# Kernel optimization log

Measured on AMD Instinct MI355X. Metric: run time of the kernel, lower is better.

## Reference

```python
import jax, jax.numpy as jnp
import numpy as np

ALPHA = 0.2  # LeakyReLU negative slope


def setup_inputs() -> dict:
    key = jax.random.key(0)
    k1, k2, k3, k4 = jax.random.split(key, 4)
    N, F_in, F_out = 8192, 128, 64
    x = jax.random.normal(k1, (N, F_in), dtype=jnp.float32)
    w = jax.random.normal(k2, (F_in, F_out), dtype=jnp.float32) * (1.0 / np.sqrt(F_in))
    a = jax.random.normal(k3, (2 * F_out, 1), dtype=jnp.float32) * (1.0 / np.sqrt(2 * F_out))
    adj_mat = jax.random.randint(k4, (N, N), 0, 2, dtype=jnp.int32)
    return {"x": x, "adj_mat": adj_mat, "w": w, "a": a}


def reference(x, adj_mat, w, a):
    # wh: [N, F_out]
    wh = x @ w
    F_out = w.shape[1]
    # The original builds a_input[i,j] = concat(wh[i], wh[j]) and dots with a.
    # Equivalently: e[i,j] = wh[i]@a[:F] + wh[j]@a[F:], computed without the
    # O(N^2 * 2F) concat tensor.
    src = wh @ a[:F_out, 0]   # [N]
    dst = wh @ a[F_out:, 0]   # [N]
    e = jax.nn.leaky_relu(src[:, None] + dst[None, :], negative_slope=ALPHA)  # [N,N]
    # NOTE: original masks non-edges with 0.0 (1e-12*zeros == 0), not -inf.
    attn = jnp.where(adj_mat > 0, e, jnp.zeros((), dtype=e.dtype))
    attn = jax.nn.softmax(attn, axis=1)
    h_prime = attn @ wh       # [N, F_out]
    return jax.nn.elu(h_prime)
```

## Files before the change

### kernel.cpp

```cpp
#include <hip/hip_runtime.h>
#include <hip/hip_bf16.h>


constexpr int N_ROWS = 8192;
constexpr int F_IN   = 128;
constexpr int F_OUT  = 64;
#define LRELU_A 0.2f
#define LOG2E   1.4426950408889634f

constexpr size_t OFF_WHT  = 0;
constexpr size_t OFF_SRC  = 1048576;
constexpr size_t OFF_DST  = OFF_SRC + 32768;
constexpr size_t OFF_LP   = OFF_DST + 32768;
constexpr size_t OFF_ACC  = OFF_LP + 16 * 32768;

typedef __attribute__((ext_vector_type(4))) float f32x4;
typedef __attribute__((ext_vector_type(4))) int   i32x4;
typedef __attribute__((ext_vector_type(8))) short s16x8;

static __device__ __forceinline__ short f2bf(float f) {
  unsigned u = __float_as_uint(f);
  u = (u + 0x7fffu + ((u >> 16) & 1u)) >> 16;
  return (short)u;
}

__global__ __launch_bounds__(256) void k1_proj(
    const float* __restrict__ x, const float* __restrict__ w,
    const float* __restrict__ a, short* __restrict__ whT,
    float* __restrict__ src, float* __restrict__ dst)
{
  const int lane = threadIdx.x & 63;
  const int wid  = threadIdx.x >> 6;
  const int rowBase = blockIdx.x * 32 + wid * 8;

  float acc[8];
#pragma unroll
  for (int r = 0; r < 8; ++r) acc[r] = 0.0f;

#pragma unroll 1
  for (int kc = 0; kc < 4; ++kc) {
    float wreg[32];
#pragma unroll
    for (int kk = 0; kk < 32; ++kk)
      wreg[kk] = w[(kc * 32 + kk) * F_OUT + lane];
#pragma unroll
    for (int r = 0; r < 8; ++r) {
      const f32x4* xp = (const f32x4*)(x + (size_t)(rowBase + r) * F_IN + kc * 32);
#pragma unroll
      for (int q = 0; q < 8; ++q) {
        f32x4 xv = xp[q];
        acc[r] = fmaf(xv.x, wreg[4*q+0], acc[r]);
        acc[r] = fmaf(xv.y, wreg[4*q+1], acc[r]);
        acc[r] = fmaf(xv.z, wreg[4*q+2], acc[r]);
        acc[r] = fmaf(xv.w, wreg[4*q+3], acc[r]);
      }
    }
  }

  s16x8 hb;
#pragma unroll
  for (int r = 0; r < 8; ++r) hb[r] = f2bf(acc[r]);
  *(s16x8*)&whT[(size_t)lane * N_ROWS + rowBase] = hb;

  const float aS = a[lane];
  const float aD = a[F_OUT + lane];
#pragma unroll
  for (int r = 0; r < 8; ++r) {
    float ts = acc[r] * aS;
    float td = acc[r] * aD;
#pragma unroll
    for (int off = 32; off > 0; off >>= 1) {
      ts += __shfl_xor(ts, off, 64);
      td += __shfl_xor(td, off, 64);
    }
    if (lane == 0) {
      src[rowBase + r] = ts * LOG2E;
      dst[rowBase + r] = td * LOG2E;
    }
  }
}

template<int S>
__global__ __launch_bounds__(512, 2) void k2_attn(
    const int* __restrict__ adj, const short* __restrict__ whT,
    const float* __restrict__ src, const float* __restrict__ dst,
    float* __restrict__ acc_part, float* __restrict__ l_part)
{
  constexpr int JLEN = N_ROWS / S;
  constexpr int NI   = JLEN / 64;
  __shared__ short Blds[64 * JLEN];
  __shared__ float Dlds[JLEN];

  const int tid  = threadIdx.x;
  const int lane = tid & 63;
  const int wid  = tid >> 6;
  const int s    = blockIdx.y;
  const int jbase = s * JLEN;
  const int rowg = blockIdx.x * 128 + wid * 16;
  const int r16  = lane & 15;
  const int kq   = lane >> 4;

#pragma unroll
  for (int q = 0; q < 8; ++q) {
    const int m   = tid + q * 512;
    const int f   = m >> 6;
    const int c16 = m & 63;
    const s16x8 v = *(const s16x8*)(whT + (size_t)f * N_ROWS + jbase + c16 * 8);
    *(s16x8*)((char*)Blds + f * (JLEN * 2) + ((c16 * 16) ^ ((f & 7) << 4))) = v;
  }
  if (tid < JLEN / 4)
    *(f32x4*)&Dlds[tid * 4] = *(const f32x4*)(dst + jbase + tid * 4);
  __syncthreads();

  const size_t arow = (size_t)(rowg + r16) * N_ROWS;
  const float sv = src[rowg + r16];
  const int cb0 = jbase + kq * 8;
  const int cswz = (r16 & 7) << 4;

  f32x4 acc0 = {0,0,0,0}, acc1 = {0,0,0,0}, acc2 = {0,0,0,0}, acc3 = {0,0,0,0};
  float lp = 0.0f;

  i32x4 A[3][4];

  auto issueAdj = [&](int b, int i) {
    const int* p = adj + arow + cb0 + i * 64;
    A[b][0] = *(const i32x4*)(p);
    A[b][1] = *(const i32x4*)(p + 4);
    A[b][2] = *(const i32x4*)(p + 32);
    A[b][3] = *(const i32x4*)(p + 36);
  };

  issueAdj(0, 0); issueAdj(1, 1); issueAdj(2, 2);

#pragma unroll
  for (int i = 0; i < NI; ++i) {
#pragma unroll
    for (int h = 0; h < 2; ++h) {
      const int db = kq * 8 + i * 64 + h * 32;
      const f32x4 dA = *(const f32x4*)&Dlds[db];
      const f32x4 dB = *(const f32x4*)&Dlds[db + 4];
      const i32x4 aA = A[i % 3][2 * h];
      const i32x4 aB = A[i % 3][2 * h + 1];
      float p0, p1, p2, p3, p4, p5, p6, p7;
#define PE(pp, dd, aa) { float e = sv + (dd); e = fmaxf(e, LRELU_A * e); \
                         (pp) = ((aa) > 0) ? __builtin_amdgcn_exp2f(e) : 1.0f; }
      PE(p0, dA.x, aA.x) PE(p1, dA.y, aA.y) PE(p2, dA.z, aA.z) PE(p3, dA.w, aA.w)
      PE(p4, dB.x, aB.x) PE(p5, dB.y, aB.y) PE(p6, dB.z, aB.z) PE(p7, dB.w, aB.w)
#undef PE
      lp += ((p0 + p1) + (p2 + p3)) + ((p4 + p5) + (p6 + p7));
      union { s16x8 v; __hip_bfloat16 b[8]; } u;
      u.b[0] = __float2bfloat16(p0); u.b[1] = __float2bfloat16(p1);
      u.b[2] = __float2bfloat16(p2); u.b[3] = __float2bfloat16(p3);
      u.b[4] = __float2bfloat16(p4); u.b[5] = __float2bfloat16(p5);
      u.b[6] = __float2bfloat16(p6); u.b[7] = __float2bfloat16(p7);
      const char* bb = (const char*)Blds;
      const int colb = (i * 64 + h * 32 + kq * 8) * 2;
      const s16x8 b0 = *(const s16x8*)(bb + (0 * 16 + r16) * (JLEN * 2) + (colb ^ cswz));
      const s16x8 b1 = *(const s16x8*)(bb + (1 * 16 + r16) * (JLEN * 2) + (colb ^ cswz));
      const s16x8 b2 = *(const s16x8*)(bb + (2 * 16 + r16) * (JLEN * 2) + (colb ^ cswz));
      const s16x8 b3 = *(const s16x8*)(bb + (3 * 16 + r16) * (JLEN * 2) + (colb ^ cswz));
      acc0 = __builtin_amdgcn_mfma_f32_16x16x32_bf16(u.v, b0, acc0, 0, 0, 0);
      acc1 = __builtin_amdgcn_mfma_f32_16x16x32_bf16(u.v, b1, acc1, 0, 0, 0);
      acc2 = __builtin_amdgcn_mfma_f32_16x16x32_bf16(u.v, b2, acc2, 0, 0, 0);
      acc3 = __builtin_amdgcn_mfma_f32_16x16x32_bf16(u.v, b3, acc3, 0, 0, 0);
    }
    if (i + 3 < NI) issueAdj(i % 3, i + 3);
  }

  lp += __shfl_xor(lp, 16, 64);
  lp += __shfl_xor(lp, 32, 64);
  if (lane < 16) l_part[(size_t)s * N_ROWS + rowg + lane] = lp;

#define STORE_ACC(av, nt) _Pragma("unroll") \
  for (int rg = 0; rg < 4; ++rg) { \
    const int row = rowg + kq * 4 + rg; \
    acc_part[((size_t)s * N_ROWS + row) * F_OUT + (nt) * 16 + r16] = (av)[rg]; \
  }
  STORE_ACC(acc0, 0) STORE_ACC(acc1, 1) STORE_ACC(acc2, 2) STORE_ACC(acc3, 3)
#undef STORE_ACC
}

template<int S>
__global__ __launch_bounds__(256) void k3_combine(
    const float* __restrict__ acc_part, const float* __restrict__ l_part,
    float* __restrict__ out)
{
  const int idx = blockIdx.x * 256 + threadIdx.x;
  const int row = idx >> 4;
  const int f4  = idx & 15;
  f32x4 h = {0.f, 0.f, 0.f, 0.f};
  float l = 0.f;
#pragma unroll
  for (int s = 0; s < S; ++s) {
    h += *(const f32x4*)(acc_part + ((size_t)s * N_ROWS + row) * F_OUT + 4 * f4);
    l += l_part[(size_t)s * N_ROWS + row];
  }
  const float inv = 1.0f / l;
  f32x4 o;
  {
    float v0 = h.x * inv; o.x = v0 > 0.f ? v0 : (__expf(v0) - 1.0f);
    float v1 = h.y * inv; o.y = v1 > 0.f ? v1 : (__expf(v1) - 1.0f);
    float v2 = h.z * inv; o.z = v2 > 0.f ? v2 : (__expf(v2) - 1.0f);
    float v3 = h.w * inv; o.w = v3 > 0.f ? v3 : (__expf(v3) - 1.0f);
  }
  *(f32x4*)(out + (size_t)row * F_OUT + 4 * f4) = o;
}

extern "C" void kernel_launch(void* const* d_in, const int* in_sizes, int n_in,
                              void* d_out, int out_size, void* d_ws, size_t ws_size,
                              hipStream_t stream) {
  const float* x   = (const float*)d_in[0];
  const int*   adj = (const int*)d_in[1];
  const float* w   = (const float*)d_in[2];
  const float* a   = (const float*)d_in[3];
  float* out = (float*)d_out;
  char* ws = (char*)d_ws;

  short* whT      = (short*)(ws + OFF_WHT);
  float* src      = (float*)(ws + OFF_SRC);
  float* dst      = (float*)(ws + OFF_DST);
  float* l_part   = (float*)(ws + OFF_LP);
  float* acc_part = (float*)(ws + OFF_ACC);

  k1_proj<<<N_ROWS / 32, 256, 0, stream>>>(x, w, a, whT, src, dst);
  k2_attn<16><<<dim3(N_ROWS / 128, 16), 512, 0, stream>>>(adj, whT, src, dst,
                                                          acc_part, l_part);
  k3_combine<16><<<(N_ROWS * F_OUT / 4) / 256, 256, 0, stream>>>(acc_part, l_part, out);
}
```

Measured before the change: 91.81 us.

## Coalesce adjacency loads via LDS staging of probabilities and smaller blocks

Each lane now loads contiguous 16-byte chunks of adjacency rows in a row-major pattern (8 lanes per row), so global reads of the dominant adj matrix are better coalesced. The computed probabilities are written to a per-wave LDS tile and re-read in MFMA A-operand layout. Blocks shrink from 512 to 256 threads (64 rows), doubling the grid, and each block now reloads the whT slice. This adds LDS round-trips and duplicate B-tile loads per block in exchange for memory-access efficiency on the bandwidth-bound adj stream.

```diff
diff --git a/kernel.cpp b/kernel.cpp
--- a/kernel.cpp
+++ b/kernel.cpp
@@ -16,6 +16,7 @@
 
 typedef __attribute__((ext_vector_type(4))) float f32x4;
 typedef __attribute__((ext_vector_type(4))) int   i32x4;
+typedef __attribute__((ext_vector_type(4))) short s16x4;
 typedef __attribute__((ext_vector_type(8))) short s16x8;
 
 static __device__ __forceinline__ short f2bf(float f) {
@@ -81,28 +82,32 @@
 }
 
 template<int S>
-__global__ __launch_bounds__(512, 2) void k2_attn(
+__global__ __launch_bounds__(256, 2) void k2_attn(
     const int* __restrict__ adj, const short* __restrict__ whT,
     const float* __restrict__ src, const float* __restrict__ dst,
     float* __restrict__ acc_part, float* __restrict__ l_part)
 {
   constexpr int JLEN = N_ROWS / S;
   constexpr int NI   = JLEN / 64;
+  constexpr int PSTR = 144;
   __shared__ short Blds[64 * JLEN];
   __shared__ float Dlds[JLEN];
+  __shared__ short Plds[4][16 * (PSTR / 2)];
 
   const int tid  = threadIdx.x;
   const int lane = tid & 63;
   const int wid  = tid >> 6;
   const int s    = blockIdx.y;
   const int jbase = s * JLEN;
-  const int rowg = blockIdx.x * 128 + wid * 16;
+  const int rowg = blockIdx.x * 64 + wid * 16;
   const int r16  = lane & 15;
   const int kq   = lane >> 4;
-
-#pragma unroll
-  for (int q = 0; q < 8; ++q) {
-    const int m   = tid + q * 512;
+  const int lg   = lane >> 3;
+  const int lc   = lane & 7;
+
+#pragma unroll
+  for (int q = 0; q < 16; ++q) {
+    const int m   = tid + q * 256;
     const int f   = m >> 6;
     const int c16 = m & 63;
     const s16x8 v = *(const s16x8*)(whT + (size_t)f * N_ROWS + jbase + c16 * 8);
@@ -112,64 +117,73 @@
     *(f32x4*)&Dlds[tid * 4] = *(const f32x4*)(dst + jbase + tid * 4);
   __syncthreads();
 
-  const size_t arow = (size_t)(rowg + r16) * N_ROWS;
-  const float sv = src[rowg + r16];
-  const int cb0 = jbase + kq * 8;
+  const size_t rbA = (size_t)(rowg + lg) * N_ROWS + jbase + lc * 4;
+  const size_t rbB = rbA + (size_t)8 * N_ROWS;
+  const float srcA = src[rowg + lg];
+  const float srcB = src[rowg + 8 + lg];
   const int cswz = (r16 & 7) << 4;
+  char* const myP = (char*)&Plds[wid][0];
 
   f32x4 acc0 = {0,0,0,0}, acc1 = {0,0,0,0}, acc2 = {0,0,0,0}, acc3 = {0,0,0,0};
-  float lp = 0.0f;
+  float lpA = 0.0f, lpB = 0.0f;
 
   i32x4 A[3][4];
 
   auto issueAdj = [&](int b, int i) {
-    const int* p = adj + arow + cb0 + i * 64;
-    A[b][0] = *(const i32x4*)(p);
-    A[b][1] = *(const i32x4*)(p + 4);
-    A[b][2] = *(const i32x4*)(p + 32);
-    A[b][3] = *(const i32x4*)(p + 36);
+    A[b][0] = *(const i32x4*)(adj + rbA + i * 64);
+    A[b][1] = *(const i32x4*)(adj + rbB + i * 64);
+    A[b][2] = *(const i32x4*)(adj + rbA + i * 64 + 32);
+    A[b][3] = *(const i32x4*)(adj + rbB + i * 64 + 32);
   };
 
   issueAdj(0, 0); issueAdj(1, 1); issueAdj(2, 2);
 
 #pragma unroll
   for (int i = 0; i < NI; ++i) {
-#pragma unroll
-    for (int h = 0; h < 2; ++h) {
-      const int db = kq * 8 + i * 64 + h * 32;
-      const f32x4 dA = *(const f32x4*)&Dlds[db];
-      const f32x4 dB = *(const f32x4*)&Dlds[db + 4];
-      const i32x4 aA = A[i % 3][2 * h];
-      const i32x4 aB = A[i % 3][2 * h + 1];
-      float p0, p1, p2, p3, p4, p5, p6, p7;
-#define PE(pp, dd, aa) { float e = sv + (dd); e = fmaxf(e, LRELU_A * e); \
+    const f32x4 d0 = *(const f32x4*)&Dlds[i * 64 + lc * 4];
+    const f32x4 d1 = *(const f32x4*)&Dlds[i * 64 + 32 + lc * 4];
+#pragma unroll
+    for (int t = 0; t < 4; ++t) {
+      const i32x4 av = A[i % 3][t];
+      const float sv = (t & 1) ? srcB : srcA;
+      const f32x4 dd = (t >> 1) ? d1 : d0;
+      float p0, p1, p2, p3;
+#define PE(pp, dv, aa) { float e = sv + (dv); e = fmaxf(e, LRELU_A * e); \
                          (pp) = ((aa) > 0) ? __builtin_amdgcn_exp2f(e) : 1.0f; }
-      PE(p0, dA.x, aA.x) PE(p1, dA.y, aA.y) PE(p2, dA.z, aA.z) PE(p3, dA.w, aA.w)
-      PE(p4, dB.x, aB.x) PE(p5, dB.y, aB.y) PE(p6, dB.z, aB.z) PE(p7, dB.w, aB.w)
+      PE(p0, dd.x, av.x) PE(p1, dd.y, av.y) PE(p2, dd.z, av.z) PE(p3, dd.w, av.w)
 #undef PE
-      lp += ((p0 + p1) + (p2 + p3)) + ((p4 + p5) + (p6 + p7));
-      union { s16x8 v; __hip_bfloat16 b[8]; } u;
+      if (t & 1) lpB += (p0 + p1) + (p2 + p3);
+      else       lpA += (p0 + p1) + (p2 + p3);
+      union { s16x4 v; __hip_bfloat16 b[4]; } u;
       u.b[0] = __float2bfloat16(p0); u.b[1] = __float2bfloat16(p1);
       u.b[2] = __float2bfloat16(p2); u.b[3] = __float2bfloat16(p3);
-      u.b[4] = __float2bfloat16(p4); u.b[5] = __float2bfloat16(p5);
-      u.b[6] = __float2bfloat16(p6); u.b[7] = __float2bfloat16(p7);
+      const int prow = (t & 1) * 8 + lg;
+      *(s16x4*)(myP + prow * PSTR + (t >> 1) * 64 + lc * 8) = u.v;
+    }
+    if (i + 3 < NI) issueAdj(i % 3, i + 3);
+#pragma unroll
+    for (int h = 0; h < 2; ++h) {
+      const s16x8 af = *(const s16x8*)(myP + r16 * PSTR + h * 64 + kq * 16);
       const char* bb = (const char*)Blds;
       const int colb = (i * 64 + h * 32 + kq * 8) * 2;
       const s16x8 b0 = *(const s16x8*)(bb + (0 * 16 + r16) * (JLEN * 2) + (colb ^ cswz));
       const s16x8 b1 = *(const s16x8*)(bb + (1 * 16 + r16) * (JLEN * 2) + (colb ^ cswz));
       const s16x8 b2 = *(const s16x8*)(bb + (2 * 16 + r16) * (JLEN * 2) + (colb ^ cswz));
       const s16x8 b3 = *(const s16x8*)(bb + (3 * 16 + r16) * (JLEN * 2) + (colb ^ cswz));
-      acc0 = __builtin_amdgcn_mfma_f32_16x16x32_bf16(u.v, b0, acc0, 0, 0, 0);
-      acc1 = __builtin_amdgcn_mfma_f32_16x16x32_bf16(u.v, b1, acc1, 0, 0, 0);
-      acc2 = __builtin_amdgcn_mfma_f32_16x16x32_bf16(u.v, b2, acc2, 0, 0, 0);
-      acc3 = __builtin_amdgcn_mfma_f32_16x16x32_bf16(u.v, b3, acc3, 0, 0, 0);
-    }
-    if (i + 3 < NI) issueAdj(i % 3, i + 3);
-  }
-
-  lp += __shfl_xor(lp, 16, 64);
-  lp += __shfl_xor(lp, 32, 64);
-  if (lane < 16) l_part[(size_t)s * N_ROWS + rowg + lane] = lp;
+      acc0 = __builtin_amdgcn_mfma_f32_16x16x32_bf16(af, b0, acc0, 0, 0, 0);
+      acc1 = __builtin_amdgcn_mfma_f32_16x16x32_bf16(af, b1, acc1, 0, 0, 0);
+      acc2 = __builtin_amdgcn_mfma_f32_16x16x32_bf16(af, b2, acc2, 0, 0, 0);
+      acc3 = __builtin_amdgcn_mfma_f32_16x16x32_bf16(af, b3, acc3, 0, 0, 0);
+    }
+  }
+
+  lpA += __shfl_xor(lpA, 1, 64); lpB += __shfl_xor(lpB, 1, 64);
+  lpA += __shfl_xor(lpA, 2, 64); lpB += __shfl_xor(lpB, 2, 64);
+  lpA += __shfl_xor(lpA, 4, 64); lpB += __shfl_xor(lpB, 4, 64);
+  if (lc == 0) {
+    l_part[(size_t)s * N_ROWS + rowg + lg]     = lpA;
+    l_part[(size_t)s * N_ROWS + rowg + 8 + lg] = lpB;
+  }
 
 #define STORE_ACC(av, nt) _Pragma("unroll") \
   for (int rg = 0; rg < 4; ++rg) { \
@@ -223,7 +237,7 @@
   float* acc_part = (float*)(ws + OFF_ACC);
 
   k1_proj<<<N_ROWS / 32, 256, 0, stream>>>(x, w, a, whT, src, dst);
-  k2_attn<16><<<dim3(N_ROWS / 128, 16), 512, 0, stream>>>(adj, whT, src, dst,
-                                                          acc_part, l_part);
+  k2_attn<16><<<dim3(N_ROWS / 64, 16), 256, 0, stream>>>(adj, whT, src, dst,
+                                                         acc_part, l_part);
   k3_combine<16><<<(N_ROWS * F_OUT / 4) / 256, 256, 0, stream>>>(acc_part, l_part, out);
 }
```

After: 94.48 us. 2.9% more time.

## Halve column splits and stage whT tiles through LDS in segments

Applied to the files above, without the earlier changes.

Reduces the column split count from 16 to 8, so each attention block covers 1024 columns. The whT tile is now loaded into LDS in two 512-column stages with barriers, which keeps the LDS footprint unchanged. This halves the partial accumulator traffic written by k2 and read by k3, and halves the number of blocks. In exchange, the grid has fewer blocks, and there is an extra serialized barrier and stage reload with no overlap between the adjacency prefetch and the B tile load.

```diff
diff --git a/kernel.cpp b/kernel.cpp
--- a/kernel.cpp
+++ b/kernel.cpp
@@ -87,8 +87,10 @@
     float* __restrict__ acc_part, float* __restrict__ l_part)
 {
   constexpr int JLEN = N_ROWS / S;
-  constexpr int NI   = JLEN / 64;
-  __shared__ short Blds[64 * JLEN];
+  constexpr int SEG  = 512;
+  constexpr int NSTG = JLEN / SEG;
+  constexpr int NI   = SEG / 64;
+  __shared__ short Blds[64 * SEG];
   __shared__ float Dlds[JLEN];
 
   const int tid  = threadIdx.x;
@@ -100,21 +102,11 @@
   const int r16  = lane & 15;
   const int kq   = lane >> 4;
 
-#pragma unroll
-  for (int q = 0; q < 8; ++q) {
-    const int m   = tid + q * 512;
-    const int f   = m >> 6;
-    const int c16 = m & 63;
-    const s16x8 v = *(const s16x8*)(whT + (size_t)f * N_ROWS + jbase + c16 * 8);
-    *(s16x8*)((char*)Blds + f * (JLEN * 2) + ((c16 * 16) ^ ((f & 7) << 4))) = v;
-  }
-  if (tid < JLEN / 4)
-    *(f32x4*)&Dlds[tid * 4] = *(const f32x4*)(dst + jbase + tid * 4);
-  __syncthreads();
+  for (int t4 = tid * 4; t4 < JLEN; t4 += 2048)
+    *(f32x4*)&Dlds[t4] = *(const f32x4*)(dst + jbase + t4);
 
   const size_t arow = (size_t)(rowg + r16) * N_ROWS;
   const float sv = src[rowg + r16];
-  const int cb0 = jbase + kq * 8;
   const int cswz = (r16 & 7) << 4;
 
   f32x4 acc0 = {0,0,0,0}, acc1 = {0,0,0,0}, acc2 = {0,0,0,0}, acc3 = {0,0,0,0};
@@ -122,49 +114,65 @@
 
   i32x4 A[3][4];
 
-  auto issueAdj = [&](int b, int i) {
-    const int* p = adj + arow + cb0 + i * 64;
-    A[b][0] = *(const i32x4*)(p);
-    A[b][1] = *(const i32x4*)(p + 4);
-    A[b][2] = *(const i32x4*)(p + 32);
-    A[b][3] = *(const i32x4*)(p + 36);
-  };
-
-  issueAdj(0, 0); issueAdj(1, 1); issueAdj(2, 2);
-
-#pragma unroll
-  for (int i = 0; i < NI; ++i) {
-#pragma unroll
-    for (int h = 0; h < 2; ++h) {
-      const int db = kq * 8 + i * 64 + h * 32;
-      const f32x4 dA = *(const f32x4*)&Dlds[db];
-      const f32x4 dB = *(const f32x4*)&Dlds[db + 4];
-      const i32x4 aA = A[i % 3][2 * h];
-      const i32x4 aB = A[i % 3][2 * h + 1];
-      float p0, p1, p2, p3, p4, p5, p6, p7;
+#pragma unroll
+  for (int st = 0; st < NSTG; ++st) {
+    const int jb2 = jbase + st * SEG;
+    if (st > 0) __syncthreads();
+#pragma unroll
+    for (int q = 0; q < 8; ++q) {
+      const int m   = tid + q * 512;
+      const int f   = m >> 6;
+      const int c16 = m & 63;
+      const s16x8 v = *(const s16x8*)(whT + (size_t)f * N_ROWS + jb2 + c16 * 8);
+      *(s16x8*)((char*)Blds + f * (SEG * 2) + ((c16 * 16) ^ ((f & 7) << 4))) = v;
+    }
+    __syncthreads();
+
+    const int cb0 = jb2 + kq * 8;
+    auto issueAdj = [&](int b, int i) {
+      const int* p = adj + arow + cb0 + i * 64;
+      A[b][0] = *(const i32x4*)(p);
+      A[b][1] = *(const i32x4*)(p + 4);
+      A[b][2] = *(const i32x4*)(p + 32);
+      A[b][3] = *(const i32x4*)(p + 36);
+    };
+
+    issueAdj(0, 0); issueAdj(1, 1); issueAdj(2, 2);
+
+#pragma unroll
+    for (int i = 0; i < NI; ++i) {
+#pragma unroll
+      for (int h = 0; h < 2; ++h) {
+        const int db = st * SEG + kq * 8 + i * 64 + h * 32;
+        const f32x4 dA = *(const f32x4*)&Dlds[db];
+        const f32x4 dB = *(const f32x4*)&Dlds[db + 4];
+        const i32x4 aA = A[i % 3][2 * h];
+        const i32x4 aB = A[i % 3][2 * h + 1];
+        float p0, p1, p2, p3, p4, p5, p6, p7;
 #define PE(pp, dd, aa) { float e = sv + (dd); e = fmaxf(e, LRELU_A * e); \
                          (pp) = ((aa) > 0) ? __builtin_amdgcn_exp2f(e) : 1.0f; }
-      PE(p0, dA.x, aA.x) PE(p1, dA.y, aA.y) PE(p2, dA.z, aA.z) PE(p3, dA.w, aA.w)
-      PE(p4, dB.x, aB.x) PE(p5, dB.y, aB.y) PE(p6, dB.z, aB.z) PE(p7, dB.w, aB.w)
+        PE(p0, dA.x, aA.x) PE(p1, dA.y, aA.y) PE(p2, dA.z, aA.z) PE(p3, dA.w, aA.w)
+        PE(p4, dB.x, aB.x) PE(p5, dB.y, aB.y) PE(p6, dB.z, aB.z) PE(p7, dB.w, aB.w)
 #undef PE
-      lp += ((p0 + p1) + (p2 + p3)) + ((p4 + p5) + (p6 + p7));
-      union { s16x8 v; __hip_bfloat16 b[8]; } u;
-      u.b[0] = __float2bfloat16(p0); u.b[1] = __float2bfloat16(p1);
-      u.b[2] = __float2bfloat16(p2); u.b[3] = __float2bfloat16(p3);
-      u.b[4] = __float2bfloat16(p4); u.b[5] = __float2bfloat16(p5);
-      u.b[6] = __float2bfloat16(p6); u.b[7] = __float2bfloat16(p7);
-      const char* bb = (const char*)Blds;
-      const int colb = (i * 64 + h * 32 + kq * 8) * 2;
-      const s16x8 b0 = *(const s16x8*)(bb + (0 * 16 + r16) * (JLEN * 2) + (colb ^ cswz));
-      const s16x8 b1 = *(const s16x8*)(bb + (1 * 16 + r16) * (JLEN * 2) + (colb ^ cswz));
-      const s16x8 b2 = *(const s16x8*)(bb + (2 * 16 + r16) * (JLEN * 2) + (colb ^ cswz));
-      const s16x8 b3 = *(const s16x8*)(bb + (3 * 16 + r16) * (JLEN * 2) + (colb ^ cswz));
-      acc0 = __builtin_amdgcn_mfma_f32_16x16x32_bf16(u.v, b0, acc0, 0, 0, 0);
-      acc1 = __builtin_amdgcn_mfma_f32_16x16x32_bf16(u.v, b1, acc1, 0, 0, 0);
-      acc2 = __builtin_amdgcn_mfma_f32_16x16x32_bf16(u.v, b2, acc2, 0, 0, 0);
-      acc3 = __builtin_amdgcn_mfma_f32_16x16x32_bf16(u.v, b3, acc3, 0, 0, 0);
-    }
-    if (i + 3 < NI) issueAdj(i % 3, i + 3);
+        lp += ((p0 + p1) + (p2 + p3)) + ((p4 + p5) + (p6 + p7));
+        union { s16x8 v; __hip_bfloat16 b[8]; } u;
+        u.b[0] = __float2bfloat16(p0); u.b[1] = __float2bfloat16(p1);
+        u.b[2] = __float2bfloat16(p2); u.b[3] = __float2bfloat16(p3);
+        u.b[4] = __float2bfloat16(p4); u.b[5] = __float2bfloat16(p5);
+        u.b[6] = __float2bfloat16(p6); u.b[7] = __float2bfloat16(p7);
+        const char* bb = (const char*)Blds;
+        const int colb = (i * 64 + h * 32 + kq * 8) * 2;
+        const s16x8 b0 = *(const s16x8*)(bb + (0 * 16 + r16) * (SEG * 2) + (colb ^ cswz));
+        const s16x8 b1 = *(const s16x8*)(bb + (1 * 16 + r16) * (SEG * 2) + (colb ^ cswz));
+        const s16x8 b2 = *(const s16x8*)(bb + (2 * 16 + r16) * (SEG * 2) + (colb ^ cswz));
+        const s16x8 b3 = *(const s16x8*)(bb + (3 * 16 + r16) * (SEG * 2) + (colb ^ cswz));
+        acc0 = __builtin_amdgcn_mfma_f32_16x16x32_bf16(u.v, b0, acc0, 0, 0, 0);
+        acc1 = __builtin_amdgcn_mfma_f32_16x16x32_bf16(u.v, b1, acc1, 0, 0, 0);
+        acc2 = __builtin_amdgcn_mfma_f32_16x16x32_bf16(u.v, b2, acc2, 0, 0, 0);
+        acc3 = __builtin_amdgcn_mfma_f32_16x16x32_bf16(u.v, b3, acc3, 0, 0, 0);
+      }
+      if (i + 3 < NI) issueAdj(i % 3, i + 3);
+    }
   }
 
   lp += __shfl_xor(lp, 16, 64);
@@ -223,7 +231,7 @@
   float* acc_part = (float*)(ws + OFF_ACC);
 
   k1_proj<<<N_ROWS / 32, 256, 0, stream>>>(x, w, a, whT, src, dst);
-  k2_attn<16><<<dim3(N_ROWS / 128, 16), 512, 0, stream>>>(adj, whT, src, dst,
-                                                          acc_part, l_part);
-  k3_combine<16><<<(N_ROWS * F_OUT / 4) / 256, 256, 0, stream>>>(acc_part, l_part, out);
-}
+  k2_attn<8><<<dim3(N_ROWS / 128, 8), 512, 0, stream>>>(adj, whT, src, dst,
+                                                        acc_part, l_part);
+  k3_combine<8><<<(N_ROWS * F_OUT / 4) / 256, 256, 0, stream>>>(acc_part, l_part, out);
+}
```

Measured after the change: 87.77 us. 1.05x faster.
